# Kernel tuning notes

Measured on AMD Instinct MI355X. Metric: run time of the kernel, lower is better.

Reference implementation:

```python
import jax, jax.numpy as jnp
import numpy as np

B, N, D = 4, 2048, 768
H, DH = 12, 64  # heads, qk/v head dim
SCALE = DH ** -0.5


def setup_inputs() -> dict:
    key = jax.random.key(0)
    ks = jax.random.split(key, 6)
    s = (1.0 / np.sqrt(D)).astype(np.float32)
    return {
        'x': jax.random.normal(ks[0], (B, N, D), dtype=jnp.float32),
        'x_mask': jax.random.randint(ks[1], (B, N), 0, 2) > 0,
        'Wq': jax.random.normal(ks[2], (D, H * DH), dtype=jnp.float32) * s,
        'Wk': jax.random.normal(ks[3], (D, H * DH), dtype=jnp.float32) * s,
        'Wv': jax.random.normal(ks[4], (D, H * DH), dtype=jnp.float32) * s,
        'Wo': jax.random.normal(ks[5], (H * DH, D), dtype=jnp.float32) * s,
    }


def reference(x, x_mask, Wq, Wk, Wv, Wo):
    # projections (no bias), split heads: b n (h d) -> b h n d
    q = (x @ Wq).reshape(B, N, H, DH).transpose(0, 2, 1, 3)
    k = (x @ Wk).reshape(B, N, H, DH).transpose(0, 2, 1, 3)
    v = (x @ Wv).reshape(B, N, H, DH).transpose(0, 2, 1, 3)
    dots = jnp.einsum('bhid,bhjd->bhij', q, k) * SCALE
    mask_value = -jnp.finfo(dots.dtype).max
    # q_mask [b,1,i,1] & k_mask [b,1,1,j] (self-attention: both from x_mask)
    input_mask = x_mask[:, None, :, None] & x_mask[:, None, None, :]
    dots = jnp.where(input_mask, dots, mask_value)
    attn = jax.nn.softmax(dots.astype(jnp.float32), axis=-1)
    # dropout is identity in eval mode
    out = jnp.einsum('bhij,bhjd->bhid', attn, v)
    out = out.transpose(0, 2, 1, 3).reshape(B, N, H * DH)  # b h n d -> b n (h d)
    return out @ Wo
```

## Files before the change

kernel.cpp:

```cpp
#include <hip/hip_runtime.h>


#define B_ 4
#define N_ 2048
#define D_ 768
#define H_ 12
#define DH_ 64
#define CSC_ 0.18033688011112042f

typedef __attribute__((ext_vector_type(8))) short bf8_t;
typedef __attribute__((ext_vector_type(4))) float f4_t;
typedef __attribute__((ext_vector_type(16))) float f16v;
typedef __attribute__((ext_vector_type(4))) int i4_t;

__device__ __forceinline__ short f2b(float f) {
  union { float f; unsigned u; } v; v.f = f;
  unsigned r = v.u + 0x7FFFu + ((v.u >> 16) & 1u);
  return (short)(r >> 16);
}
__device__ __forceinline__ unsigned cvtpk(float lo, float hi) {
  unsigned r;
  asm("v_cvt_pk_bf16_f32 %0, %1, %2" : "=v"(r) : "v"(lo), "v"(hi));
  return r;
}
__device__ __forceinline__ void plswap(unsigned& a, unsigned& b) {
  asm("v_permlane32_swap_b32 %0, %1" : "+v"(a), "+v"(b));
}
__device__ __forceinline__ float max3f(float a, float b, float c) {
  float r;
  asm("v_max3_f32 %0, %1, %2, %3" : "=v"(r) : "v"(a), "v"(b), "v"(c));
  return r;
}

#define GLOAD_LDS16(gp, lp)                                                       \
  __builtin_amdgcn_global_load_lds(                                               \
      (const __attribute__((address_space(1))) void*)(gp),                        \
      (__attribute__((address_space(3))) void*)(lp), 16, 0, 0)

__global__ __launch_bounds__(256) void k_maskidx(const int* __restrict__ xmask,
                                                 int* __restrict__ idx,
                                                 int* __restrict__ cnt) {
  int b = blockIdx.x, t = threadIdx.x;
  const int* mp = xmask + b * N_;
  int loc[8], c = 0;
#pragma unroll
  for (int j = 0; j < 8; ++j) {
    int n = t * 8 + j;
    if (mp[n]) loc[c++] = n;
  }
  __shared__ int sc[256];
  sc[t] = c;
  __syncthreads();
  for (int off = 1; off < 256; off <<= 1) {
    int v = (t >= off) ? sc[t - off] : 0;
    __syncthreads();
    sc[t] += v;
    __syncthreads();
  }
  int base = sc[t] - c;
  int* op = idx + b * N_;
  for (int j = 0; j < c; ++j) op[base + j] = loc[j];
  if (t == 255) cnt[b] = sc[255];
}

__global__ __launch_bounds__(256) void k_xsumA(const float* __restrict__ x,
                                               float* __restrict__ xpart) {
  int b = blockIdx.y, ch = blockIdx.x, t = threadIdx.x;
  const float* xp = x + ((size_t)b * N_ + ch * 32) * D_;
  float a0 = 0, a1 = 0, a2 = 0;
  for (int r = 0; r < 32; ++r) {
    const float* rp = xp + (size_t)r * D_;
    a0 += rp[t]; a1 += rp[t + 256]; a2 += rp[t + 512];
  }
  float* op = xpart + ((size_t)b * 64 + ch) * D_;
  op[t] = a0; op[t + 256] = a1; op[t + 512] = a2;
}

__global__ __launch_bounds__(256) void k_xmean(const float* __restrict__ xpart,
                                               float* __restrict__ xmean) {
  int b = blockIdx.y;
  int col = blockIdx.x * 64 + (threadIdx.x & 63);
  int grp = threadIdx.x >> 6;
  float s = 0;
#pragma unroll
  for (int i = 0; i < 16; ++i)
    s += xpart[((size_t)b * 64 + grp * 16 + i) * D_ + col];
  __shared__ float red[4][64];
  red[grp][threadIdx.x & 63] = s;
  __syncthreads();
  if (grp == 0) {
    int cl = threadIdx.x & 63;
    xmean[b * D_ + col] = (red[0][cl] + red[1][cl] + red[2][cl] + red[3][cl]) * (1.f / 2048.f);
  }
}

__global__ __launch_bounds__(256) void k_gemv(const float* __restrict__ xv,
                                              const float* __restrict__ W,
                                              float* __restrict__ y) {
  int b = blockIdx.y;
  int cl = threadIdx.x & 63;
  int col = blockIdx.x * 64 + cl;
  int grp = threadIdx.x >> 6;
  __shared__ float xs[768];
  for (int c = threadIdx.x; c < 768; c += 256) xs[c] = xv[b * D_ + c];
  __syncthreads();
  float acc = 0;
  const float* wp = W + (size_t)(grp * 192) * D_ + col;
  const float* xp = xs + grp * 192;
#pragma unroll 4
  for (int k = 0; k < 192; ++k) acc += xp[k] * wp[(size_t)k * D_];
  __shared__ float red[4][64];
  red[grp][cl] = acc;
  __syncthreads();
  if (grp == 0) y[b * D_ + col] = red[0][cl] + red[1][cl] + red[2][cl] + red[3][cl];
}

__global__ __launch_bounds__(256) void k_gatherx(const float* __restrict__ x,
                                                 const int* __restrict__ idx,
                                                 const int* __restrict__ cnt,
                                                 short* __restrict__ xc) {
  int b = blockIdx.y;
  int j = blockIdx.x * 8 + (threadIdx.x >> 5);
  int cn = cnt[b];
  int l5 = threadIdx.x & 31;
  short* op = xc + ((size_t)b * N_ + j) * D_;
  if (j < cn) {
    int n = idx[b * N_ + j];
    const float* rp = x + ((size_t)b * N_ + n) * D_;
#pragma unroll
    for (int it = 0; it < 3; ++it) {
      int c = (l5 + it * 32) * 8;
      float4 v0 = *(const float4*)(rp + c);
      float4 v1 = *(const float4*)(rp + c + 4);
      bf8_t o;
      o[0] = f2b(v0.x); o[1] = f2b(v0.y); o[2] = f2b(v0.z); o[3] = f2b(v0.w);
      o[4] = f2b(v1.x); o[5] = f2b(v1.y); o[6] = f2b(v1.z); o[7] = f2b(v1.w);
      *(bf8_t*)(op + c) = o;
    }
  } else {
    const bf8_t zz = {0, 0, 0, 0, 0, 0, 0, 0};
#pragma unroll
    for (int it = 0; it < 3; ++it) {
      int c = (l5 + it * 32) * 8;
      *(bf8_t*)(op + c) = zz;
    }
  }
}

__global__ __launch_bounds__(256) void k_wtrans(const float* __restrict__ Wq,
                                                const float* __restrict__ Wk,
                                                const float* __restrict__ Wv,
                                                const float* __restrict__ Wo,
                                                short* __restrict__ WqkvT,
                                                short* __restrict__ WoT) {
  int z = blockIdx.z;
  const float* W = (z == 0) ? Wq : (z == 1) ? Wk : (z == 2) ? Wv : Wo;
  short* dst = (z < 3) ? (WqkvT + (size_t)z * D_ * D_) : WoT;
  float sc = (z == 0) ? CSC_ : 1.f;
  __shared__ float T[64][65];
  int r0 = blockIdx.y * 64, c0 = blockIdx.x * 64;
  int tr = threadIdx.x >> 6, tc = threadIdx.x & 63;
#pragma unroll
  for (int i = 0; i < 16; ++i) {
    int r = tr + i * 4;
    T[r][tc] = W[(size_t)(r0 + r) * D_ + c0 + tc];
  }
  __syncthreads();
#pragma unroll
  for (int i = 0; i < 16; ++i) {
    int r = tr + i * 4;
    dst[(size_t)(c0 + r) * D_ + r0 + tc] = f2b(T[tc][r] * sc);
  }
}

template <int MODE>
__global__ __launch_bounds__(256) void k_gemm(const short* __restrict__ A,
                                              const short* __restrict__ BT, int K,
                                              short* __restrict__ Qb, short* __restrict__ Kb,
                                              short* __restrict__ Vb,
                                              float* __restrict__ Cout, int ldc,
                                              const int* __restrict__ cnt,
                                              const int* __restrict__ idx) {
  __shared__ short As[2][128 * 64];
  __shared__ short Bs[2][128 * 64];
  int gx = gridDim.x, gy = gridDim.y;
  int nwg = gx * gy;
  int flat = blockIdx.y * gx + blockIdx.x;
  int cpx = nwg >> 3;
  int swzb = (flat & 7) * cpx + (flat >> 3);
  int row0 = (swzb % gy) * 128, col0 = (swzb / gy) * 128;

  int bb = row0 >> 11;
  int cn = cnt[bb];
  int cnpad = (cn + 127) & ~127;
  if ((row0 & 2047) >= cnpad) return;

  int tid = threadIdx.x, lane = tid & 63, w = tid >> 6;
  int wr = w >> 1, wc = w & 1;
  int lr = lane & 15, lhi = lane >> 4;
  f4_t acc[4][4];
#pragma unroll
  for (int mi = 0; mi < 4; ++mi)
#pragma unroll
    for (int ni = 0; ni < 4; ++ni) acc[mi][ni] = (f4_t){0.f, 0.f, 0.f, 0.f};

  int sub = lane >> 3;
  int scb = ((lane & 7) * 16) ^ (sub << 4);
  auto STAGE = [&](int k0, int buf) {
    char* ab = (char*)As[buf] + (w << 12);
    char* bb2 = (char*)Bs[buf] + (w << 12);
#pragma unroll
    for (int i = 0; i < 4; ++i) {
      int r = 32 * w + 8 * i + sub;
      GLOAD_LDS16((const char*)(A + (size_t)(row0 + r) * K + k0) + scb, ab + (i << 10));
      GLOAD_LDS16((const char*)(BT + (size_t)(col0 + r) * K + k0) + scb, bb2 + (i << 10));
    }
  };

  STAGE(0, 0);

  int nt = K / 64;
  for (int t = 0; t < nt; ++t) {
    int cur = t & 1;
    if (t + 1 < nt) {
      STAGE((t + 1) * 64, cur ^ 1);
      asm volatile("s_waitcnt vmcnt(8)" ::: "memory");
    } else {
      asm volatile("s_waitcnt vmcnt(0)" ::: "memory");
    }
    __builtin_amdgcn_sched_barrier(0);
    __builtin_amdgcn_s_barrier();

    const char* Ac = (const char*)As[cur];
    const char* Bc = (const char*)Bs[cur];
    int rsw = (lr & 7) << 4;
#pragma unroll
    for (int kc = 0; kc < 2; ++kc) {
      bf8_t av[4], bv[4];
#pragma unroll
      for (int mi = 0; mi < 4; ++mi) {
        int row = 64 * wr + 16 * mi + lr;
        av[mi] = *(const bf8_t*)(Ac + row * 128 + ((64 * kc + 16 * lhi) ^ rsw));
      }
#pragma unroll
      for (int ni = 0; ni < 4; ++ni) {
        int row = 64 * wc + 16 * ni + lr;
        bv[ni] = *(const bf8_t*)(Bc + row * 128 + ((64 * kc + 16 * lhi) ^ rsw));
      }
#pragma unroll
      for (int mi = 0; mi < 4; ++mi)
#pragma unroll
        for (int ni = 0; ni < 4; ++ni)
          acc[mi][ni] = __builtin_amdgcn_mfma_f32_16x16x32_bf16(av[mi], bv[ni], acc[mi][ni], 0, 0, 0);
    }
    __builtin_amdgcn_sched_barrier(0);
    __builtin_amdgcn_s_barrier();
  }

#pragma unroll
  for (int mi = 0; mi < 4; ++mi)
#pragma unroll
    for (int ni = 0; ni < 4; ++ni)
#pragma unroll
      for (int r = 0; r < 4; ++r) {
        int row = row0 + 64 * wr + 16 * mi + 4 * lhi + r;
        int col = col0 + 64 * wc + 16 * ni + lr;
        float v = acc[mi][ni][r];
        if (MODE == 0) {
          int which = col / 768;
          int cc2 = col - which * 768;
          int h = cc2 >> 6, dh = cc2 & 63;
          int b = row >> 11, n = row & 2047;
          size_t dst = (((size_t)(b * H_ + h)) * N_ + n) * DH_ + dh;
          short bv2 = f2b(v);
          if (which == 0) Qb[dst] = bv2;
          else if (which == 1) Kb[dst] = bv2;
          else Vb[dst] = bv2;
        } else {
          int j = row & 2047;
          if (j < cn) {
            int n = idx[(row & ~2047) + j];
            Cout[((size_t)(row & ~2047) + n) * ldc + col] = v;
          }
        }
      }
}

__global__ __launch_bounds__(256) void k_vtrans(const short* __restrict__ V,
                                                const int* __restrict__ cnt,
                                                short* __restrict__ Vt) {
  int bh = blockIdx.y, b = bh / H_;
  int n0 = blockIdx.x * 64;
  int cn = cnt[b];
  int cnpad = (cn + 127) & ~127;
  if (n0 >= cnpad) return;
  __shared__ short T[64][72];
  int tr = threadIdx.x >> 6, tc = threadIdx.x & 63;
  const short* Vp = V + (size_t)bh * N_ * DH_;
  short* Vtp = Vt + (size_t)bh * DH_ * N_;
#pragma unroll
  for (int i = 0; i < 16; ++i) {
    int r = tr + i * 4;
    T[r][tc] = Vp[(size_t)(n0 + r) * DH_ + tc];
  }
  __syncthreads();
#pragma unroll
  for (int i = 0; i < 16; ++i) {
    int r = tr + i * 4;
    Vtp[(size_t)r * N_ + n0 + tc] = T[tc][r];
  }
}

__global__ __launch_bounds__(256) void k_fillout(const int* __restrict__ xmask,
                                                 const float* __restrict__ outrowG,
                                                 float* __restrict__ out) {
  int b = blockIdx.y;
  int n = blockIdx.x * 32 + (threadIdx.x >> 3);
  int cg = threadIdx.x & 7;
  if (xmask[b * N_ + n]) return;
  const float* rp = outrowG + b * D_;
  float* op = out + ((size_t)b * N_ + n) * D_;
#pragma unroll
  for (int it = 0; it < 12; ++it) {
    int c = cg * 8 + it * 64;
    float4 v0 = *(const float4*)(rp + c);
    float4 v1 = *(const float4*)(rp + c + 4);
    *(float4*)(op + c) = v0;
    *(float4*)(op + c + 4) = v1;
  }
}

__global__ __launch_bounds__(256, 3) void k_attn(const short* __restrict__ Q,
                                                 const short* __restrict__ Kcg,
                                                 const short* __restrict__ Vtcg,
                                                 const int* __restrict__ cnt,
                                                 short* __restrict__ Aout) {
  int bh = blockIdx.y;
  int b = bh / H_, h = bh - b * H_;
  int cn = cnt[b];
  int nqt = (cn + 127) >> 7;
  if ((int)blockIdx.x >= nqt) return;
  int nkt = (cn + 63) >> 6;
  const short* Qp = Q + (size_t)bh * N_ * DH_;
  const short* Kp = Kcg + (size_t)bh * N_ * DH_;
  const short* Vp = Vtcg + (size_t)bh * DH_ * N_;
  int q0 = blockIdx.x * 128;
  int tid = threadIdx.x, lane = tid & 63, w = tid >> 6;
  int lq = lane & 31, hi = lane >> 5;

  __shared__ char smem[32768];

  int qrow = q0 + 32 * w + lq;

  bf8_t qf[4];
#pragma unroll
  for (int kc = 0; kc < 4; ++kc)
    qf[kc] = *(const bf8_t*)(Qp + (size_t)qrow * DH_ + 16 * kc + 8 * hi);

  short NEGBIG = f2b(-1e30f);
  bf8_t qbf = {hi ? (short)0 : (short)0x3F80, 0, 0, 0, 0, 0, 0, 0};

  f16v acco[2];
#pragma unroll
  for (int i = 0; i < 16; ++i) { acco[0][i] = 0.f; acco[1][i] = 0.f; }
  float m = -1e29f, lsum = 0.f;

  auto STAGE = [&](int key0, int buf) {
    char* kb_ = smem + buf * 16384;
    char* vb_ = kb_ + 8192;
    int row = tid >> 3;
    int cb = (tid & 7) * 16;
    char* lk = kb_ + ((tid >> 6) << 10);
    char* lv = vb_ + ((tid >> 6) << 10);
#pragma unroll
    for (int rr = 0; rr < 2; ++rr) {
      int r2 = row + rr * 32;
      int sw = cb ^ ((r2 & 7) << 4);
      GLOAD_LDS16((const char*)(Kp + (size_t)(key0 + r2) * DH_) + sw, lk + rr * 4096);
      GLOAD_LDS16((const char*)(Vp + (size_t)r2 * N_ + key0) + sw, lv + rr * 4096);
    }
  };

  STAGE(0, 0);
  __syncthreads();

  for (int kt = 0; kt < nkt; ++kt) {
    int cur = kt & 1;
    if (kt + 1 < nkt) STAGE((kt + 1) * 64, cur ^ 1);

    const char* kbase = smem + cur * 16384;
    const char* vbase = kbase + 8192;
    int key0 = kt * 64;

    f16v accs[2];
#pragma unroll
    for (int i = 0; i < 16; ++i) { accs[0][i] = 0.f; accs[1][i] = 0.f; }
    int swz = (lq & 7) << 4;
    __builtin_amdgcn_s_setprio(1);
#pragma unroll
    for (int kc = 0; kc < 4; ++kc) {
      int colb = (32 * kc + 16 * hi) ^ swz;
      bf8_t k0 = *(const bf8_t*)(kbase + lq * 128 + colb);
      bf8_t k1 = *(const bf8_t*)(kbase + (32 + lq) * 128 + colb);
      accs[0] = __builtin_amdgcn_mfma_f32_32x32x16_bf16(k0, qf[kc], accs[0], 0, 0, 0);
      accs[1] = __builtin_amdgcn_mfma_f32_32x32x16_bf16(k1, qf[kc], accs[1], 0, 0, 0);
    }
    __builtin_amdgcn_s_setprio(0);
    if (key0 + 64 > cn) {
      bf8_t bf0 = {(hi || key0 + lq < cn) ? (short)0 : NEGBIG, 0, 0, 0, 0, 0, 0, 0};
      bf8_t bf1 = {(hi || key0 + 32 + lq < cn) ? (short)0 : NEGBIG, 0, 0, 0, 0, 0, 0, 0};
      accs[0] = __builtin_amdgcn_mfma_f32_32x32x16_bf16(bf0, qbf, accs[0], 0, 0, 0);
      accs[1] = __builtin_amdgcn_mfma_f32_32x32x16_bf16(bf1, qbf, accs[1], 0, 0, 0);
    }

    float mx = max3f(accs[0][0], accs[0][1], accs[0][2]);
#pragma unroll
    for (int i = 3; i < 15; i += 2) mx = max3f(mx, accs[0][i], accs[0][i + 1]);
    mx = max3f(mx, accs[0][15], accs[1][0]);
#pragma unroll
    for (int i = 1; i < 15; i += 2) mx = max3f(mx, accs[1][i], accs[1][i + 1]);
    mx = fmaxf(mx, accs[1][15]);
    mx = fmaxf(mx, __shfl_xor(mx, 32));
    if (!__all(mx <= m + 8.f)) {
      float mnew = fmaxf(m, mx);
      float sc = __builtin_amdgcn_exp2f(m - mnew);
      m = mnew;
      lsum *= sc;
#pragma unroll
      for (int i = 0; i < 16; ++i) { acco[0][i] *= sc; acco[1][i] *= sc; }
    }
    float psa[4] = {0.f, 0.f, 0.f, 0.f};
#pragma unroll
    for (int kb2 = 0; kb2 < 2; ++kb2)
#pragma unroll
      for (int r = 0; r < 16; ++r) {
        float p = __builtin_amdgcn_exp2f(accs[kb2][r] - m);
        accs[kb2][r] = p;
        psa[r & 3] += p;
      }
    float ps = (psa[0] + psa[1]) + (psa[2] + psa[3]);
    ps += __shfl_xor(ps, 32);
    lsum += ps;

    __builtin_amdgcn_s_setprio(1);
#pragma unroll
    for (int kc = 0; kc < 4; ++kc) {
      int kb2 = kc >> 1, rb = (kc & 1) * 8;
      unsigned a_ = cvtpk(accs[kb2][rb + 0], accs[kb2][rb + 1]);
      unsigned b_ = cvtpk(accs[kb2][rb + 4], accs[kb2][rb + 5]);
      unsigned c_ = cvtpk(accs[kb2][rb + 2], accs[kb2][rb + 3]);
      unsigned d_ = cvtpk(accs[kb2][rb + 6], accs[kb2][rb + 7]);
      plswap(a_, b_);
      plswap(c_, d_);
      union { i4_t i; bf8_t v; } pu;
      pu.i = (i4_t){(int)a_, (int)c_, (int)b_, (int)d_};
      int colb = (32 * kc + 16 * hi) ^ swz;
      bf8_t v0 = *(const bf8_t*)(vbase + lq * 128 + colb);
      bf8_t v1 = *(const bf8_t*)(vbase + (32 + lq) * 128 + colb);
      acco[0] = __builtin_amdgcn_mfma_f32_32x32x16_bf16(v0, pu.v, acco[0], 0, 0, 0);
      acco[1] = __builtin_amdgcn_mfma_f32_32x32x16_bf16(v1, pu.v, acco[1], 0, 0, 0);
    }
    __builtin_amdgcn_s_setprio(0);

    __syncthreads();
  }
  __syncthreads();

  float inv = 1.f / lsum;
  unsigned* Os = (unsigned*)smem + w * 1152;
#pragma unroll
  for (int dhb = 0; dhb < 2; ++dhb)
#pragma unroll
    for (int r = 0; r < 16; r += 2) {
      unsigned pk = cvtpk(acco[dhb][r] * inv, acco[dhb][r + 1] * inv);
      int colu = 16 * dhb + ((r & 3) >> 1) + 4 * (r >> 2) + 2 * hi;
      Os[lq * 36 + colu] = pk;
    }
#pragma unroll
  for (int it = 0; it < 4; ++it) {
    int q = (lane >> 3) + 8 * it;
    int qr2 = q0 + 32 * w + q;
    if (qr2 < cn) {
      i4_t vv = *(const i4_t*)(Os + q * 36 + 4 * (lane & 7));
      union { i4_t i; bf8_t s; } u2;
      u2.i = vv;
      size_t off = ((size_t)b * N_ + qr2) * D_ + h * DH_ + 8 * (lane & 7);
      *(bf8_t*)(Aout + off) = u2.s;
    }
  }
}

extern "C" void kernel_launch(void* const* d_in, const int* in_sizes, int n_in,
                              void* d_out, int out_size, void* d_ws, size_t ws_size,
                              hipStream_t stream) {
  (void)in_sizes; (void)n_in; (void)out_size; (void)ws_size;
  const float* x  = (const float*)d_in[0];
  const int*   xm = (const int*)d_in[1];
  const float* Wq = (const float*)d_in[2];
  const float* Wk = (const float*)d_in[3];
  const float* Wv = (const float*)d_in[4];
  const float* Wo = (const float*)d_in[5];
  float* out = (float*)d_out;
  char* ws = (char*)d_ws;

  short* xc      = (short*)(ws + 0);
  short* Ao      = (short*)(ws + 0);
  short* WqkvT   = (short*)(ws + 12582912);
  short* WoT     = (short*)(ws + 16121856);
  int*   idxb    = (int*)(ws + 17301504);
  int*   cntb    = (int*)(ws + 17334272);
  float* xpart   = (float*)(ws + 17334528);
  float* vmeanG  = (float*)(ws + 18120960);
  float* outrowG = (float*)(ws + 18133248);
  float* xmeanG  = (float*)(ws + 18145536);
  short* Qb      = (short*)(ws + 18874368);
  short* Kc      = (short*)(ws + 31457280);
  short* Vc      = (short*)(ws + 44040192);
  short* Vtc     = (short*)(ws + 56623104);

  k_maskidx<<<4, 256, 0, stream>>>(xm, idxb, cntb);
  k_xsumA<<<dim3(64, 4), 256, 0, stream>>>(x, xpart);
  k_gatherx<<<dim3(256, 4), 256, 0, stream>>>(x, idxb, cntb, xc);
  k_wtrans<<<dim3(12, 12, 4), 256, 0, stream>>>(Wq, Wk, Wv, Wo, WqkvT, WoT);
  k_gemm<0><<<dim3(18, 64), 256, 0, stream>>>(xc, WqkvT, 768, Qb, Kc, Vc,
                                              nullptr, 0, cntb, nullptr);
  k_vtrans<<<dim3(32, 48), 256, 0, stream>>>(Vc, cntb, Vtc);
  k_xmean<<<dim3(12, 4), 256, 0, stream>>>(xpart, xmeanG);
  k_gemv<<<dim3(12, 4), 256, 0, stream>>>(xmeanG, Wv, vmeanG);
  k_gemv<<<dim3(12, 4), 256, 0, stream>>>(vmeanG, Wo, outrowG);
  k_attn<<<dim3(16, 48), 256, 0, stream>>>(Qb, Kc, Vtc, cntb, Ao);
  k_fillout<<<dim3(64, 4), 256, 0, stream>>>(xm, outrowG, out);
  k_gemm<1><<<dim3(6, 64), 256, 0, stream>>>(Ao, WoT, 768, nullptr, nullptr, nullptr,
                                             out, 768, cntb, idxb);
}
```

Measured before the change: 163.2 us.

## Fuse x gather into row-sum kernel and simplify GEMM staging to register prefetch

Adds an inverse position map in the mask kernel so the x column-sum kernel can also write bf16 compacted rows, removing the separate gather kernel and a second read of x. An extra block per batch zero-fills only the padding rows, instead of every row past the count. The GEMM swaps its double-buffered direct global-to-LDS loads with XOR swizzle for a single padded LDS buffer fed through register prefetch and two syncthreads per tile. The GEMM change reduces LDS use but loses the async double buffering and adds barriers. The fused kernel's bf16 stores are scalar shorts rather than 16-byte vectors.

```diff
diff --git a/kernel.cpp b/kernel.cpp
--- a/kernel.cpp
+++ b/kernel.cpp
@@ -39,15 +39,13 @@
 
 __global__ __launch_bounds__(256) void k_maskidx(const int* __restrict__ xmask,
                                                  int* __restrict__ idx,
+                                                 int* __restrict__ pos,
                                                  int* __restrict__ cnt) {
   int b = blockIdx.x, t = threadIdx.x;
   const int* mp = xmask + b * N_;
-  int loc[8], c = 0;
-#pragma unroll
-  for (int j = 0; j < 8; ++j) {
-    int n = t * 8 + j;
-    if (mp[n]) loc[c++] = n;
-  }
+  int c = 0;
+#pragma unroll
+  for (int j = 0; j < 8; ++j) c += (mp[t * 8 + j] != 0);
   __shared__ int sc[256];
   sc[t] = c;
   __syncthreads();
@@ -57,23 +55,46 @@
     sc[t] += v;
     __syncthreads();
   }
-  int base = sc[t] - c;
-  int* op = idx + b * N_;
-  for (int j = 0; j < c; ++j) op[base + j] = loc[j];
+  int p = sc[t] - c;
+#pragma unroll
+  for (int j = 0; j < 8; ++j) {
+    int n = t * 8 + j;
+    int v = mp[n];
+    pos[b * N_ + n] = v ? p : -1;
+    if (v) { idx[b * N_ + p] = n; ++p; }
+  }
   if (t == 255) cnt[b] = sc[255];
 }
 
-__global__ __launch_bounds__(256) void k_xsumA(const float* __restrict__ x,
-                                               float* __restrict__ xpart) {
+__global__ __launch_bounds__(256) void k_gxsum(const float* __restrict__ x,
+                                               const int* __restrict__ pos,
+                                               const int* __restrict__ cnt,
+                                               float* __restrict__ xpart,
+                                               short* __restrict__ xc) {
   int b = blockIdx.y, ch = blockIdx.x, t = threadIdx.x;
+  if (ch == 64) {
+    int cn = cnt[b], cnpad = (cn + 127) & ~127;
+    int nel = (cnpad - cn) * D_;
+    short* base = xc + ((size_t)b * N_ + cn) * D_;
+    const bf8_t zz = {0, 0, 0, 0, 0, 0, 0, 0};
+    for (int i = t * 8; i < nel; i += 256 * 8) *(bf8_t*)(base + i) = zz;
+    return;
+  }
   const float* xp = x + ((size_t)b * N_ + ch * 32) * D_;
+  const int* pp = pos + b * N_ + ch * 32;
   float a0 = 0, a1 = 0, a2 = 0;
   for (int r = 0; r < 32; ++r) {
     const float* rp = xp + (size_t)r * D_;
-    a0 += rp[t]; a1 += rp[t + 256]; a2 += rp[t + 512];
-  }
-  float* op = xpart + ((size_t)b * 64 + ch) * D_;
-  op[t] = a0; op[t + 256] = a1; op[t + 512] = a2;
+    float v0 = rp[t], v1 = rp[t + 256], v2 = rp[t + 512];
+    a0 += v0; a1 += v1; a2 += v2;
+    int p = pp[r];
+    if (p >= 0) {
+      short* op = xc + ((size_t)b * N_ + p) * D_;
+      op[t] = f2b(v0); op[t + 256] = f2b(v1); op[t + 512] = f2b(v2);
+    }
+  }
+  float* op2 = xpart + ((size_t)b * 64 + ch) * D_;
+  op2[t] = a0; op2[t + 256] = a1; op2[t + 512] = a2;
 }
 
 __global__ __launch_bounds__(256) void k_xmean(const float* __restrict__ xpart,
@@ -113,38 +134,6 @@
   red[grp][cl] = acc;
   __syncthreads();
   if (grp == 0) y[b * D_ + col] = red[0][cl] + red[1][cl] + red[2][cl] + red[3][cl];
-}
-
-__global__ __launch_bounds__(256) void k_gatherx(const float* __restrict__ x,
-                                                 const int* __restrict__ idx,
-                                                 const int* __restrict__ cnt,
-                                                 short* __restrict__ xc) {
-  int b = blockIdx.y;
-  int j = blockIdx.x * 8 + (threadIdx.x >> 5);
-  int cn = cnt[b];
-  int l5 = threadIdx.x & 31;
-  short* op = xc + ((size_t)b * N_ + j) * D_;
-  if (j < cn) {
-    int n = idx[b * N_ + j];
-    const float* rp = x + ((size_t)b * N_ + n) * D_;
-#pragma unroll
-    for (int it = 0; it < 3; ++it) {
-      int c = (l5 + it * 32) * 8;
-      float4 v0 = *(const float4*)(rp + c);
-      float4 v1 = *(const float4*)(rp + c + 4);
-      bf8_t o;
-      o[0] = f2b(v0.x); o[1] = f2b(v0.y); o[2] = f2b(v0.z); o[3] = f2b(v0.w);
-      o[4] = f2b(v1.x); o[5] = f2b(v1.y); o[6] = f2b(v1.z); o[7] = f2b(v1.w);
-      *(bf8_t*)(op + c) = o;
-    }
-  } else {
-    const bf8_t zz = {0, 0, 0, 0, 0, 0, 0, 0};
-#pragma unroll
-    for (int it = 0; it < 3; ++it) {
-      int c = (l5 + it * 32) * 8;
-      *(bf8_t*)(op + c) = zz;
-    }
-  }
 }
 
 __global__ __launch_bounds__(256) void k_wtrans(const float* __restrict__ Wq,
@@ -181,8 +170,8 @@
                                               float* __restrict__ Cout, int ldc,
                                               const int* __restrict__ cnt,
                                               const int* __restrict__ idx) {
-  __shared__ short As[2][128 * 64];
-  __shared__ short Bs[2][128 * 64];
+  __shared__ short As[128 * 72];
+  __shared__ short Bs[128 * 72];
   int gx = gridDim.x, gy = gridDim.y;
   int nwg = gx * gy;
   int flat = blockIdx.y * gx + blockIdx.x;
@@ -204,57 +193,58 @@
 #pragma unroll
     for (int ni = 0; ni < 4; ++ni) acc[mi][ni] = (f4_t){0.f, 0.f, 0.f, 0.f};
 
-  int sub = lane >> 3;
-  int scb = ((lane & 7) * 16) ^ (sub << 4);
-  auto STAGE = [&](int k0, int buf) {
-    char* ab = (char*)As[buf] + (w << 12);
-    char* bb2 = (char*)Bs[buf] + (w << 12);
-#pragma unroll
-    for (int i = 0; i < 4; ++i) {
-      int r = 32 * w + 8 * i + sub;
-      GLOAD_LDS16((const char*)(A + (size_t)(row0 + r) * K + k0) + scb, ab + (i << 10));
-      GLOAD_LDS16((const char*)(BT + (size_t)(col0 + r) * K + k0) + scb, bb2 + (i << 10));
-    }
-  };
-
-  STAGE(0, 0);
+  bf8_t ra[4], rb[4];
+
+#pragma unroll
+  for (int cc = 0; cc < 4; ++cc) {
+    int c = tid + cc * 256, r = c >> 3, c8 = (c & 7) * 8;
+    ra[cc] = *(const bf8_t*)(A + (size_t)(row0 + r) * K + c8);
+    rb[cc] = *(const bf8_t*)(BT + (size_t)(col0 + r) * K + c8);
+  }
+#pragma unroll
+  for (int cc = 0; cc < 4; ++cc) {
+    int c = tid + cc * 256, r = c >> 3, c8 = (c & 7) * 8;
+    *(bf8_t*)(As + r * 72 + c8) = ra[cc];
+    *(bf8_t*)(Bs + r * 72 + c8) = rb[cc];
+  }
+  __syncthreads();
 
   int nt = K / 64;
   for (int t = 0; t < nt; ++t) {
-    int cur = t & 1;
     if (t + 1 < nt) {
-      STAGE((t + 1) * 64, cur ^ 1);
-      asm volatile("s_waitcnt vmcnt(8)" ::: "memory");
-    } else {
-      asm volatile("s_waitcnt vmcnt(0)" ::: "memory");
-    }
-    __builtin_amdgcn_sched_barrier(0);
-    __builtin_amdgcn_s_barrier();
-
-    const char* Ac = (const char*)As[cur];
-    const char* Bc = (const char*)Bs[cur];
-    int rsw = (lr & 7) << 4;
+      int k0 = (t + 1) * 64;
+#pragma unroll
+      for (int cc = 0; cc < 4; ++cc) {
+        int c = tid + cc * 256, r = c >> 3, c8 = (c & 7) * 8;
+        ra[cc] = *(const bf8_t*)(A + (size_t)(row0 + r) * K + k0 + c8);
+        rb[cc] = *(const bf8_t*)(BT + (size_t)(col0 + r) * K + k0 + c8);
+      }
+    }
 #pragma unroll
     for (int kc = 0; kc < 2; ++kc) {
       bf8_t av[4], bv[4];
 #pragma unroll
-      for (int mi = 0; mi < 4; ++mi) {
-        int row = 64 * wr + 16 * mi + lr;
-        av[mi] = *(const bf8_t*)(Ac + row * 128 + ((64 * kc + 16 * lhi) ^ rsw));
-      }
-#pragma unroll
-      for (int ni = 0; ni < 4; ++ni) {
-        int row = 64 * wc + 16 * ni + lr;
-        bv[ni] = *(const bf8_t*)(Bc + row * 128 + ((64 * kc + 16 * lhi) ^ rsw));
-      }
+      for (int mi = 0; mi < 4; ++mi)
+        av[mi] = *(const bf8_t*)(As + (64 * wr + 16 * mi + lr) * 72 + kc * 32 + lhi * 8);
+#pragma unroll
+      for (int ni = 0; ni < 4; ++ni)
+        bv[ni] = *(const bf8_t*)(Bs + (64 * wc + 16 * ni + lr) * 72 + kc * 32 + lhi * 8);
 #pragma unroll
       for (int mi = 0; mi < 4; ++mi)
 #pragma unroll
         for (int ni = 0; ni < 4; ++ni)
           acc[mi][ni] = __builtin_amdgcn_mfma_f32_16x16x32_bf16(av[mi], bv[ni], acc[mi][ni], 0, 0, 0);
     }
-    __builtin_amdgcn_sched_barrier(0);
-    __builtin_amdgcn_s_barrier();
+    __syncthreads();
+    if (t + 1 < nt) {
+#pragma unroll
+      for (int cc = 0; cc < 4; ++cc) {
+        int c = tid + cc * 256, r = c >> 3, c8 = (c & 7) * 8;
+        *(bf8_t*)(As + r * 72 + c8) = ra[cc];
+        *(bf8_t*)(Bs + r * 72 + c8) = rb[cc];
+      }
+      __syncthreads();
+    }
   }
 
 #pragma unroll
@@ -513,14 +503,14 @@
   float* vmeanG  = (float*)(ws + 18120960);
   float* outrowG = (float*)(ws + 18133248);
   float* xmeanG  = (float*)(ws + 18145536);
+  int*   posb    = (int*)(ws + 18157824);
   short* Qb      = (short*)(ws + 18874368);
   short* Kc      = (short*)(ws + 31457280);
   short* Vc      = (short*)(ws + 44040192);
   short* Vtc     = (short*)(ws + 56623104);
 
-  k_maskidx<<<4, 256, 0, stream>>>(xm, idxb, cntb);
-  k_xsumA<<<dim3(64, 4), 256, 0, stream>>>(x, xpart);
-  k_gatherx<<<dim3(256, 4), 256, 0, stream>>>(x, idxb, cntb, xc);
+  k_maskidx<<<4, 256, 0, stream>>>(xm, idxb, posb, cntb);
+  k_gxsum<<<dim3(65, 4), 256, 0, stream>>>(x, posb, cntb, xpart, xc);
   k_wtrans<<<dim3(12, 12, 4), 256, 0, stream>>>(Wq, Wk, Wv, Wo, WqkvT, WoT);
   k_gemm<0><<<dim3(18, 64), 256, 0, stream>>>(xc, WqkvT, 768, Qb, Kc, Vc,
                                               nullptr, 0, cntb, nullptr);
```

After: 174.5 us. 6.9% more time.
